# Kernel tuning notes

Hardware: AMD Instinct MI355X
Metric: run time of the kernel (lower is better)

The kernel has to match this reference:

```python
import jax, jax.numpy as jnp
import numpy as np

B, SD, SS = 2, 2048, 1024
H, NH, DH, FF = 768, 12, 64, 3072
L, V, P, NS, WIN = 6, 50265, 256, 32, 256


def layer_norm(x, g, b, eps=1e-5):
    m = x.mean(-1, keepdims=True)
    v = ((x - m) ** 2).mean(-1, keepdims=True)
    return (x - m) * jax.lax.rsqrt(v + eps) * g + b


def sliding_window_attention(q, k, v, key_mask, w):
    # q,k,v: [B,NH,S,DH]; key_mask: [B,S] (1 = attend); one-sided window w
    b, nh, s, d = q.shape
    nc = s // w
    qc = q.reshape(b, nh, nc, w, d)
    kp = jnp.pad(k, ((0, 0), (0, 0), (w, w), (0, 0)))
    vp = jnp.pad(v, ((0, 0), (0, 0), (w, w), (0, 0)))
    idx = jnp.arange(nc)[:, None] * w + jnp.arange(3 * w)[None, :]  # [nc,3w]
    kc = kp[:, :, idx]  # [B,NH,nc,3w,DH]
    vc = vp[:, :, idx]
    km = jnp.pad(key_mask, ((0, 0), (w, w)))[:, idx]  # [B,nc,3w]
    scores = jnp.einsum('bhcqd,bhckd->bhcqk', qc, kc) / np.float32(np.sqrt(d))
    rel = jnp.arange(3 * w)[None, :] - jnp.arange(w)[:, None]
    band = (rel >= 0) & (rel <= 2 * w)  # |j - i| <= w in global coords
    mask = band[None, None, None] & (km[:, None, :, None, :] > 0)
    probs = jax.nn.softmax(jnp.where(mask, scores, -1e9), axis=-1)
    return jnp.einsum('bhcqk,bhckd->bhcqd', probs, vc).reshape(b, nh, s, d)


def encode(ids, amask, word_emb, pos_emb, emb_g, emb_b, Wq, bq, Wk, bk, Wv, bv, Wo, bo,
           lnag, lnab, Wf1, bf1, Wf2, bf2, lnfg, lnfb):
    bb, s = ids.shape
    x = word_emb[ids] + pos_emb[:s][None]
    x = layer_norm(x, emb_g, emb_b)
    km = amask.astype(jnp.float32)
    for l in range(L):
        to_heads = lambda t: t.reshape(bb, s, NH, DH).transpose(0, 2, 1, 3)
        q = to_heads(x @ Wq[l] + bq[l])
        k = to_heads(x @ Wk[l] + bk[l])
        v = to_heads(x @ Wv[l] + bv[l])
        a = sliding_window_attention(q, k, v, km, WIN)
        a = a.transpose(0, 2, 1, 3).reshape(bb, s, H) @ Wo[l] + bo[l]
        x = layer_norm(x + a, lnag[l], lnab[l])
        h = jax.nn.gelu(x @ Wf1[l] + bf1[l], approximate=False) @ Wf2[l] + bf2[l]
        x = layer_norm(x + h, lnfg[l], lnfb[l])
    return x


def process_spans(seq_out, span_masks, pool_w, pj_g1, pj_b1, pj_W1, pj_c1, pj_g2, pj_b2, pj_W2, pj_c2):
    scores = jnp.clip(seq_out @ pool_w, -100.0, 100.0)  # [N,S]
    am = (span_masks == 1).astype(jnp.float32)
    scores = scores * am + (-1e9) * (1.0 - am)
    attn = jax.nn.softmax(scores, axis=-1)[..., None]
    emb = (seq_out * attn).sum(axis=1)  # [N,H]
    h = layer_norm(emb, pj_g1, pj_b1)
    h = jax.nn.gelu(h @ pj_W1 + pj_c1, approximate=False)
    h = layer_norm(h, pj_g2, pj_b2)
    proj = h @ pj_W2 + pj_c2
    n = jnp.maximum(jnp.linalg.norm(proj, axis=1, keepdims=True), 1e-12)
    return proj / n


def setup_inputs():
    key = jax.random.key(0)
    ks = jax.random.split(key, 40)
    nrm = lambda k, shape, s=0.02: (jax.random.normal(k, shape) * s).astype(jnp.float32)
    return {
        'doc_input_ids': jax.random.randint(ks[0], (B, SD), 0, V),
        'doc_attention_mask': jnp.ones((B, SD), jnp.int32),
        'summary_input_ids': jax.random.randint(ks[1], (B, SS), 0, V),
        'summary_attention_mask': jnp.ones((B, SS), jnp.int32),
        'og_span_masks': jax.random.randint(ks[2], (NS, SD), 0, 2),
        'llm_span_masks': jax.random.randint(ks[3], (NS, SS), 0, 2),
        'sample_indices': jax.random.randint(ks[4], (NS,), 0, B),
        'word_emb': nrm(ks[5], (V, H)),
        'pos_emb': nrm(ks[6], (SD, H)),
        'emb_g': jnp.ones((H,), jnp.float32), 'emb_b': jnp.zeros((H,), jnp.float32),
        'Wq': nrm(ks[7], (L, H, H)), 'bq': jnp.zeros((L, H), jnp.float32),
        'Wk': nrm(ks[8], (L, H, H)), 'bk': jnp.zeros((L, H), jnp.float32),
        'Wv': nrm(ks[9], (L, H, H)), 'bv': jnp.zeros((L, H), jnp.float32),
        'Wo': nrm(ks[10], (L, H, H)), 'bo': jnp.zeros((L, H), jnp.float32),
        'lnag': jnp.ones((L, H), jnp.float32), 'lnab': jnp.zeros((L, H), jnp.float32),
        'Wf1': nrm(ks[11], (L, H, FF)), 'bf1': jnp.zeros((L, FF), jnp.float32),
        'Wf2': nrm(ks[12], (L, FF, H)), 'bf2': jnp.zeros((L, H), jnp.float32),
        'lnfg': jnp.ones((L, H), jnp.float32), 'lnfb': jnp.zeros((L, H), jnp.float32),
        'pool_w': nrm(ks[13], (H,), 0.005),
        'pj_g1': jnp.ones((H,), jnp.float32), 'pj_b1': jnp.zeros((H,), jnp.float32),
        'pj_W1': nrm(ks[14], (H, H), 0.005), 'pj_c1': jnp.zeros((H,), jnp.float32),
        'pj_g2': jnp.ones((H,), jnp.float32), 'pj_b2': jnp.zeros((H,), jnp.float32),
        'pj_W2': nrm(ks[15], (H, P), 0.005), 'pj_c2': jnp.zeros((P,), jnp.float32),
    }


def reference(doc_input_ids, doc_attention_mask, summary_input_ids, summary_attention_mask,
              og_span_masks, llm_span_masks, sample_indices,
              word_emb, pos_emb, emb_g, emb_b, Wq, bq, Wk, bk, Wv, bv, Wo, bo,
              lnag, lnab, Wf1, bf1, Wf2, bf2, lnfg, lnfb,
              pool_w, pj_g1, pj_b1, pj_W1, pj_c1, pj_g2, pj_b2, pj_W2, pj_c2):
    enc = lambda ids, am: encode(ids, am, word_emb, pos_emb, emb_g, emb_b, Wq, bq, Wk, bk,
                                 Wv, bv, Wo, bo, lnag, lnab, Wf1, bf1, Wf2, bf2, lnfg, lnfb)
    doc_out = enc(doc_input_ids, doc_attention_mask)
    sum_out = enc(summary_input_ids, summary_attention_mask)
    human_seq = doc_out[sample_indices]  # [NS,SD,H]
    llm_seq = sum_out[sample_indices]    # [NS,SS,H]
    pj = (pool_w, pj_g1, pj_b1, pj_W1, pj_c1, pj_g2, pj_b2, pj_W2, pj_c2)
    human = process_spans(human_seq, og_span_masks, *pj)
    llm = process_spans(llm_seq, llm_span_masks, *pj)
    return (human, llm)
```

## Files before the change

### kernel.cpp

```cpp
#include <hip/hip_runtime.h>
#include <math.h>

#define BB 2
#define SDOC 2048
#define SSUM 1024
#define HD 768
#define NHEAD 12
#define DHEAD 64
#define FFD 3072
#define NLAYER 6
#define PD 256
#define NSPAN 32
#define WINSZ 256
#define QKVN 2304
#define MTOT 6144
#define KSPLIT 16

typedef short s16x8 __attribute__((ext_vector_type(8)));
typedef float f32x4 __attribute__((ext_vector_type(4)));

#define LDS_PTR(p) ((__attribute__((address_space(3))) void*)(p))
#define GLB_PTR(p) ((const __attribute__((address_space(1))) void*)(p))

__device__ __forceinline__ unsigned short f2bf(float f) {
  unsigned int u = __builtin_bit_cast(unsigned int, f);
  unsigned int r = (u + 0x7fffu + ((u >> 16) & 1u)) >> 16;
  return (unsigned short)r;
}
__device__ __forceinline__ float bf2f(unsigned short h) {
  unsigned int u = ((unsigned int)h) << 16;
  return __builtin_bit_cast(float, u);
}

__device__ __forceinline__ float gelu_f(float x) {
  float t = x * (0.7978845608f + 0.0356774081f * x * x);
  float e = __expf(2.f * t);
  float th = 1.f - 2.f / (e + 1.f);
  return 0.5f * x * (1.f + th);
}

__device__ __forceinline__ float wave_reduce_sum(float v) {
#pragma unroll
  for (int m = 32; m > 0; m >>= 1) v += __shfl_xor(v, m, 64);
  return v;
}
__device__ __forceinline__ float wave_reduce_max(float v) {
#pragma unroll
  for (int m = 32; m > 0; m >>= 1) v = fmaxf(v, __shfl_xor(v, m, 64));
  return v;
}

__device__ __forceinline__ float block_reduce_sum(float v) {
  __shared__ float s[4];
  v = wave_reduce_sum(v);
  int wave = threadIdx.x >> 6;
  if ((threadIdx.x & 63) == 0) s[wave] = v;
  __syncthreads();
  float r = (s[0] + s[1]) + (s[2] + s[3]);
  __syncthreads();
  return r;
}

__device__ __forceinline__ float block_reduce_max(float v) {
  __shared__ float s[4];
  v = wave_reduce_max(v);
  int wave = threadIdx.x >> 6;
  if ((threadIdx.x & 63) == 0) s[wave] = v;
  __syncthreads();
  float r = fmaxf(fmaxf(s[0], s[1]), fmaxf(s[2], s[3]));
  __syncthreads();
  return r;
}

__device__ __forceinline__ void block_reduce_sum2(float& a, float& b) {
  __shared__ float sa[4], sb[4];
#pragma unroll
  for (int m = 32; m > 0; m >>= 1) {
    a += __shfl_xor(a, m, 64);
    b += __shfl_xor(b, m, 64);
  }
  int wave = threadIdx.x >> 6;
  if ((threadIdx.x & 63) == 0) { sa[wave] = a; sb[wave] = b; }
  __syncthreads();
  a = (sa[0] + sa[1]) + (sa[2] + sa[3]);
  b = (sb[0] + sb[1]) + (sb[2] + sb[3]);
  __syncthreads();
}

__global__ __launch_bounds__(256) void embed_ln_kernel(
    const int* __restrict__ ids, const float* __restrict__ we, const float* __restrict__ pe,
    const float* __restrict__ g, const float* __restrict__ bt, float* __restrict__ xout,
    unsigned short* __restrict__ xb, int S) {
  int row = blockIdx.x;
  int s = row % S;
  int id = ids[row];
  int tid = threadIdx.x;
  float vals[3];
  float sum = 0.f, sq = 0.f;
#pragma unroll
  for (int i = 0; i < 3; i++) {
    int h = tid + i * 256;
    float t = we[(size_t)id * HD + h] + pe[(size_t)s * HD + h];
    vals[i] = t;
    sum += t;
    sq += t * t;
  }
  block_reduce_sum2(sum, sq);
  float mean = sum * (1.f / HD);
  float var = fmaxf(sq * (1.f / HD) - mean * mean, 0.f);
  float inv = rsqrtf(var + 1e-5f);
#pragma unroll
  for (int i = 0; i < 3; i++) {
    int h = tid + i * 256;
    float v = (vals[i] - mean) * inv * g[h] + bt[h];
    size_t off = (size_t)row * HD + h;
    xout[off] = v;
    xb[off] = f2bf(v);
  }
}

__global__ __launch_bounds__(256) void ln_kernel(
    const float* __restrict__ a, const float* __restrict__ res,
    const float* __restrict__ g, const float* __restrict__ bt, float* __restrict__ out,
    unsigned short* __restrict__ ob) {
  int row = blockIdx.x;
  int tid = threadIdx.x;
  const float* ar = a + (size_t)row * HD;
  const float* rr = res ? res + (size_t)row * HD : nullptr;
  float vals[3];
  float sum = 0.f, sq = 0.f;
#pragma unroll
  for (int i = 0; i < 3; i++) {
    int h = tid + i * 256;
    float t = ar[h] + (rr ? rr[h] : 0.f);
    vals[i] = t;
    sum += t;
    sq += t * t;
  }
  block_reduce_sum2(sum, sq);
  float mean = sum * (1.f / HD);
  float var = fmaxf(sq * (1.f / HD) - mean * mean, 0.f);
  float inv = rsqrtf(var + 1e-5f);
#pragma unroll
  for (int i = 0; i < 3; i++) {
    int h = tid + i * 256;
    float v = (vals[i] - mean) * inv * g[h] + bt[h];
    size_t off = (size_t)row * HD + h;
    out[off] = v;
    if (ob) ob[off] = f2bf(v);
  }
}

__global__ __launch_bounds__(256) void tc_cast_kernel(
    const float* __restrict__ Wq, const float* __restrict__ Wk, const float* __restrict__ Wv,
    const float* __restrict__ Wo, const float* __restrict__ Wf1, const float* __restrict__ Wf2,
    unsigned short* __restrict__ ob) {
  __shared__ float tile[32][33];
  int z = blockIdx.z;
  const float* W;
  int Kd, Nd;
  size_t off;
  switch (z) {
    case 0: W = Wq;  Kd = HD;  Nd = HD;  off = 0;        break;
    case 1: W = Wk;  Kd = HD;  Nd = HD;  off = 589824;   break;
    case 2: W = Wv;  Kd = HD;  Nd = HD;  off = 1179648;  break;
    case 3: W = Wo;  Kd = HD;  Nd = HD;  off = 1769472;  break;
    case 4: W = Wf1; Kd = HD;  Nd = FFD; off = 2359296;  break;
    default: W = Wf2; Kd = FFD; Nd = HD; off = 4718592;  break;
  }
  int tiles_n = Nd >> 5, tiles_k = Kd >> 5;
  int t = blockIdx.x;
  if (t >= tiles_n * tiles_k) return;
  int tn = t % tiles_n, tk = t / tiles_n;
  int n0 = tn * 32, k0 = tk * 32;
  int tid = threadIdx.x;
  int c = tid & 31, r0 = tid >> 5;
#pragma unroll
  for (int j = 0; j < 4; j++) {
    int r = r0 + j * 8;
    tile[r][c] = W[(size_t)(k0 + r) * Nd + n0 + c];
  }
  __syncthreads();
#pragma unroll
  for (int j = 0; j < 4; j++) {
    int r = r0 + j * 8;
    ob[off + (size_t)(n0 + r) * Kd + k0 + c] = f2bf(tile[c][r]);
  }
}

template <int TN>
__global__ __launch_bounds__(256) void gemm_mfma_t(
    const unsigned short* __restrict__ A, const unsigned short* __restrict__ B,
    const float* __restrict__ b0, const float* __restrict__ b1, const float* __restrict__ b2,
    int seg, float* __restrict__ C, unsigned short* __restrict__ Oh,
    int M, int N, int K, int act) {
  constexpr int JT = TN / 32;
  __shared__ __align__(16) unsigned short sA[2][128 * 32];
  __shared__ __align__(16) unsigned short sB[2][TN * 32];
  int tid = threadIdx.x;
  int bm = blockIdx.y * 128, bn = blockIdx.x * TN;
  int wave = tid >> 6, lane = tid & 63;
  int quad = lane >> 4, l16 = lane & 15;
  int wm = (wave >> 1) * 64, wn = (wave & 1) * (TN / 2);

  f32x4 zero = {0.f, 0.f, 0.f, 0.f};
  f32x4 acc[4][JT];
#pragma unroll
  for (int i = 0; i < 4; i++)
#pragma unroll
    for (int j = 0; j < JT; j++) acc[i][j] = zero;

  int e0 = tid * 8;
  int row0 = e0 >> 5;
  int kk0 = e0 & 31;

  auto issue = [&](int kb, int buf) {
    int k0 = kb * 32;
#pragma unroll
    for (int r = 0; r < 2; r++) {
      int row = row0 + r * 64;
      int le = (r * 256 + tid) * 8;
      size_t ga = (size_t)(bm + row) * K + k0 + kk0;
      __builtin_amdgcn_global_load_lds(GLB_PTR(A + ga), LDS_PTR(&sA[buf][le]), 16, 0, 0);
    }
#pragma unroll
    for (int r = 0; r < TN / 64; r++) {
      int row = row0 + r * 64;
      int le = (r * 256 + tid) * 8;
      size_t gb = (size_t)(bn + row) * K + k0 + kk0;
      __builtin_amdgcn_global_load_lds(GLB_PTR(B + gb), LDS_PTR(&sB[buf][le]), 16, 0, 0);
    }
  };

  int nk = K >> 5;
  issue(0, 0);
  for (int kb = 0; kb < nk; kb++) {
    __syncthreads();
    if (kb + 1 < nk) issue(kb + 1, (kb + 1) & 1);
    int buf = kb & 1;
    s16x8 af[4], bf[JT];
#pragma unroll
    for (int i = 0; i < 4; i++)
      af[i] = *(const s16x8*)&sA[buf][(wm + i * 16 + l16) * 32 + quad * 8];
#pragma unroll
    for (int j = 0; j < JT; j++)
      bf[j] = *(const s16x8*)&sB[buf][(wn + j * 16 + l16) * 32 + quad * 8];
#pragma unroll
    for (int i = 0; i < 4; i++)
#pragma unroll
      for (int j = 0; j < JT; j++)
        acc[i][j] = __builtin_amdgcn_mfma_f32_16x16x32_bf16(af[i], bf[j], acc[i][j], 0, 0, 0);
  }

#pragma unroll
  for (int j = 0; j < JT; j++) {
    int col = bn + wn + j * 16 + l16;
    int bidx = col / seg;
    int boff = col - bidx * seg;
    const float* bp = bidx == 0 ? b0 : (bidx == 1 ? b1 : b2);
    float bv = bp[boff];
#pragma unroll
    for (int i = 0; i < 4; i++) {
#pragma unroll
      for (int r = 0; r < 4; r++) {
        int rowg = bm + wm + i * 16 + quad * 4 + r;
        float v = acc[i][j][r] + bv;
        if (act == 1) v = gelu_f(v);
        size_t off = (size_t)rowg * N + col;
        if (C) C[off] = v;
        if (Oh) Oh[off] = f2bf(v);
      }
    }
  }
}

__global__ __launch_bounds__(256) void gemm_ps_kernel(
    const float* __restrict__ A, const float* __restrict__ W,
    float* __restrict__ part, int N, int K) {
  int n = blockIdx.x * 256 + threadIdx.x;
  int m = blockIdx.y;
  int M = gridDim.y;
  int ks = blockIdx.z;
  int kc = K / KSPLIT;
  int k0 = ks * kc;
  const float* ar = A + (size_t)m * K + k0;
  const float* wr = W + (size_t)k0 * N + n;
  float a0 = 0.f, a1 = 0.f, a2 = 0.f, a3 = 0.f;
  for (int k = 0; k < kc; k += 4) {
    a0 += ar[k]     * wr[(size_t)k * N];
    a1 += ar[k + 1] * wr[(size_t)(k + 1) * N];
    a2 += ar[k + 2] * wr[(size_t)(k + 2) * N];
    a3 += ar[k + 3] * wr[(size_t)(k + 3) * N];
  }
  part[((size_t)ks * M + m) * N + n] = (a0 + a1) + (a2 + a3);
}

__global__ __launch_bounds__(256) void gemm_reduce_kernel(
    const float* __restrict__ part, const float* __restrict__ bias,
    float* __restrict__ C, int N, int act) {
  int n = blockIdx.x * 256 + threadIdx.x;
  int m = blockIdx.y;
  int M = gridDim.y;
  float s = 0.f;
#pragma unroll
  for (int ks = 0; ks < KSPLIT; ks++) s += part[((size_t)ks * M + m) * N + n];
  s += bias[n];
  if (act == 1) s = gelu_f(s);
  C[(size_t)m * N + n] = s;
}

#define AQT 64
__global__ __launch_bounds__(256) void attn_mfma(
    const unsigned short* __restrict__ qkv, const int* __restrict__ amask,
    unsigned short* __restrict__ Oh, int S) {
  __shared__ unsigned short Vs[64][72];
  __shared__ unsigned short Ps[4][16][72];
  int b = blockIdx.z, hd = blockIdx.y;
  int p0 = blockIdx.x * AQT;
  int tid = threadIdx.x;
  int wave = tid >> 6, lane = tid & 63;
  int quad = lane >> 4, l16 = lane & 15;
  int kstart = p0 - WINSZ;
  const unsigned short* base = qkv + (size_t)(b * S) * QKVN + hd * DHEAD;

  s16x8 aq[2];
  {
    const unsigned short* qrow = base + (size_t)(p0 + wave * 16 + l16) * QKVN;
    aq[0] = *(const s16x8*)(qrow + quad * 8);
    aq[1] = *(const s16x8*)(qrow + 32 + quad * 8);
  }
  f32x4 o[4];
  f32x4 zero = {0.f, 0.f, 0.f, 0.f};
#pragma unroll
  for (int i = 0; i < 4; i++) o[i] = zero;
  float mi[4] = {-1e30f, -1e30f, -1e30f, -1e30f};
  float li[4] = {0.f, 0.f, 0.f, 0.f};

  for (int t = 0; t < 9; t++) {
    __syncthreads();
    {
      int key = tid & 63, d0 = (tid >> 6) * 16;
      int kp = kstart + t * 64 + key;
      if (kp >= 0 && kp < S) {
        const unsigned short* vrow = base + (size_t)kp * QKVN + 2 * HD + d0;
        s16x8 v0 = *(const s16x8*)(vrow);
        s16x8 v1 = *(const s16x8*)(vrow + 8);
#pragma unroll
        for (int j = 0; j < 8; j++) Vs[d0 + j][key] = (unsigned short)v0[j];
#pragma unroll
        for (int j = 0; j < 8; j++) Vs[d0 + 8 + j][key] = (unsigned short)v1[j];
      } else {
#pragma unroll
        for (int j = 0; j < 16; j++) Vs[d0 + j][key] = 0;
      }
    }
    __syncthreads();

    f32x4 sc[4];
#pragma unroll
    for (int nt = 0; nt < 4; nt++) {
      int kr = kstart + t * 64 + nt * 16 + l16;
      s16x8 bk0 = {0, 0, 0, 0, 0, 0, 0, 0}, bk1 = bk0;
      if (kr >= 0 && kr < S) {
        const unsigned short* krow = base + (size_t)kr * QKVN + HD;
        bk0 = *(const s16x8*)(krow + quad * 8);
        bk1 = *(const s16x8*)(krow + 32 + quad * 8);
      }
      sc[nt] = __builtin_amdgcn_mfma_f32_16x16x32_bf16(aq[0], bk0, zero, 0, 0, 0);
      sc[nt] = __builtin_amdgcn_mfma_f32_16x16x32_bf16(aq[1], bk1, sc[nt], 0, 0, 0);
    }

    float s_val[4][4];
    float tm[4] = {-1e30f, -1e30f, -1e30f, -1e30f};
#pragma unroll
    for (int nt = 0; nt < 4; nt++) {
      int j = t * 64 + nt * 16 + l16;
      int kp = kstart + j;
      int am = (kp >= 0 && kp < S) ? amask[b * S + kp] : 0;
#pragma unroll
      for (int r = 0; r < 4; r++) {
        int ql = wave * 16 + quad * 4 + r;
        bool valid = (am != 0) && (j >= ql) && (j <= ql + 512);
        float v = valid ? sc[nt][r] * 0.125f : -1e9f;
        s_val[nt][r] = v;
        tm[r] = fmaxf(tm[r], v);
      }
    }
#pragma unroll
    for (int m = 1; m < 16; m <<= 1)
#pragma unroll
      for (int r = 0; r < 4; r++) tm[r] = fmaxf(tm[r], __shfl_xor(tm[r], m, 16));

    float alpha[4], rs[4];
#pragma unroll
    for (int r = 0; r < 4; r++) {
      float mn = fmaxf(mi[r], tm[r]);
      alpha[r] = __expf(mi[r] - mn);
      mi[r] = mn;
      rs[r] = 0.f;
    }
#pragma unroll
    for (int nt = 0; nt < 4; nt++)
#pragma unroll
      for (int r = 0; r < 4; r++) {
        float p = __expf(s_val[nt][r] - mi[r]);
        rs[r] += p;
        Ps[wave][quad * 4 + r][nt * 16 + l16] = f2bf(p);
      }
#pragma unroll
    for (int m = 1; m < 16; m <<= 1)
#pragma unroll
      for (int r = 0; r < 4; r++) rs[r] += __shfl_xor(rs[r], m, 16);
#pragma unroll
    for (int r = 0; r < 4; r++) li[r] = li[r] * alpha[r] + rs[r];
#pragma unroll
    for (int dn = 0; dn < 4; dn++)
#pragma unroll
      for (int r = 0; r < 4; r++) o[dn][r] *= alpha[r];

#pragma unroll
    for (int ks = 0; ks < 2; ks++) {
      s16x8 ap = *(const s16x8*)&Ps[wave][l16][ks * 32 + quad * 8];
#pragma unroll
      for (int dn = 0; dn < 4; dn++) {
        s16x8 bv = *(const s16x8*)&Vs[dn * 16 + l16][ks * 32 + quad * 8];
        o[dn] = __builtin_amdgcn_mfma_f32_16x16x32_bf16(ap, bv, o[dn], 0, 0, 0);
      }
    }
  }

#pragma unroll
  for (int r = 0; r < 4; r++) {
    float inv = 1.f / li[r];
    int rowg = b * S + p0 + wave * 16 + quad * 4 + r;
#pragma unroll
    for (int dn = 0; dn < 4; dn++) {
      Oh[(size_t)rowg * HD + hd * DHEAD + dn * 16 + l16] = f2bf(o[dn][r] * inv);
    }
  }
}

__global__ __launch_bounds__(256) void dots_kernel(
    const float* __restrict__ x, const float* __restrict__ pw, float* __restrict__ dots) {
  int row = blockIdx.x * 4 + (threadIdx.x >> 6);
  int lane = threadIdx.x & 63;
  const float* r = x + (size_t)row * HD;
  float s = 0.f;
  for (int i = lane; i < HD; i += 64) s += r[i] * pw[i];
#pragma unroll
  for (int m = 32; m > 0; m >>= 1) s += __shfl_xor(s, m, 64);
  if (lane == 0) dots[row] = fminf(fmaxf(s, -100.f), 100.f);
}

__global__ __launch_bounds__(256) void span_softmax_kernel(
    const float* __restrict__ dots, const int* __restrict__ og_spans,
    const int* __restrict__ llm_spans, const int* __restrict__ sidx,
    float* __restrict__ probs) {
  int ns = blockIdx.x;
  int pass = ns >> 5;
  int sp = ns & 31;
  int S = pass ? SSUM : SDOC;
  const int* spans = pass ? llm_spans : og_spans;
  int rowbase = pass ? BB * SDOC : 0;
  int bi = sidx[sp];
  const float* dr = dots + rowbase + bi * S;
  int tid = threadIdx.x;
  float mx = -1e30f;
  for (int s = tid; s < S; s += 256) {
    float v = (spans[sp * S + s] == 1) ? dr[s] : -1e9f;
    mx = fmaxf(mx, v);
  }
  mx = block_reduce_max(mx);
  float sum = 0.f;
  for (int s = tid; s < S; s += 256) {
    float v = (spans[sp * S + s] == 1) ? dr[s] : -1e9f;
    float e = __expf(v - mx);
    probs[ns * SDOC + s] = e;
    sum += e;
  }
  sum = block_reduce_sum(sum);
  float inv = 1.f / sum;
  for (int s = tid; s < S; s += 256) probs[ns * SDOC + s] *= inv;
}

__global__ __launch_bounds__(256) void wsum_kernel(
    const float* __restrict__ seq, const float* __restrict__ probs,
    const int* __restrict__ sidx, float* __restrict__ pooled, int S, int ns0) {
  __shared__ float ps[256];
  int sp = blockIdx.y;
  int ns = ns0 + sp;
  int s0 = blockIdx.x * 256;
  int bi = sidx[sp];
  int tid = threadIdx.x;
  ps[tid] = probs[ns * SDOC + s0 + tid];
  __syncthreads();
  const float* xb = seq + ((size_t)bi * S + s0) * HD;
  float a0 = 0.f, a1 = 0.f, a2 = 0.f;
  for (int s = 0; s < 256; s++) {
    float p = ps[s];
    const float* row = xb + (size_t)s * HD;
    a0 += p * row[tid];
    a1 += p * row[tid + 256];
    a2 += p * row[tid + 512];
  }
  atomicAdd(&pooled[ns * HD + tid], a0);
  atomicAdd(&pooled[ns * HD + tid + 256], a1);
  atomicAdd(&pooled[ns * HD + tid + 512], a2);
}

__global__ __launch_bounds__(256) void norm_out_kernel(
    const float* __restrict__ proj, float* __restrict__ out) {
  int ns = blockIdx.x;
  float v = proj[ns * PD + threadIdx.x];
  float ss = block_reduce_sum(v * v);
  float n = fmaxf(sqrtf(ss), 1e-12f);
  out[ns * PD + threadIdx.x] = v / n;
}

static void launch_gemm128(const unsigned short* A, const unsigned short* B,
                           const float* b0, const float* b1, const float* b2, int seg,
                           float* C, unsigned short* Oh, int M, int N, int K, int act,
                           hipStream_t stream) {
  dim3 grid(N / 128, M / 128);
  gemm_mfma_t<128><<<grid, 256, 0, stream>>>(A, B, b0, b1, b2, seg, C, Oh, M, N, K, act);
}

#define WOFF_QKV 0
#define WOFF_O   1769472
#define WOFF_F1  2359296
#define WOFF_F2  4718592

extern "C" void kernel_launch(void* const* d_in, const int* in_sizes, int n_in,
                              void* d_out, int out_size, void* d_ws, size_t ws_size,
                              hipStream_t stream) {
  const int* doc_ids   = (const int*)d_in[0];
  const int* doc_am    = (const int*)d_in[1];
  const int* sum_ids   = (const int*)d_in[2];
  const int* sum_am    = (const int*)d_in[3];
  const int* og_spans  = (const int*)d_in[4];
  const int* llm_spans = (const int*)d_in[5];
  const int* sidx      = (const int*)d_in[6];
  const float* word_emb = (const float*)d_in[7];
  const float* pos_emb  = (const float*)d_in[8];
  const float* emb_g = (const float*)d_in[9];
  const float* emb_b = (const float*)d_in[10];
  const float* Wq = (const float*)d_in[11];
  const float* bq = (const float*)d_in[12];
  const float* Wk = (const float*)d_in[13];
  const float* bk = (const float*)d_in[14];
  const float* Wv = (const float*)d_in[15];
  const float* bv = (const float*)d_in[16];
  const float* Wo = (const float*)d_in[17];
  const float* bo = (const float*)d_in[18];
  const float* lnag = (const float*)d_in[19];
  const float* lnab = (const float*)d_in[20];
  const float* Wf1 = (const float*)d_in[21];
  const float* bf1 = (const float*)d_in[22];
  const float* Wf2 = (const float*)d_in[23];
  const float* bf2 = (const float*)d_in[24];
  const float* lnfg = (const float*)d_in[25];
  const float* lnfb = (const float*)d_in[26];
  const float* pool_w = (const float*)d_in[27];
  const float* pj_g1 = (const float*)d_in[28];
  const float* pj_b1 = (const float*)d_in[29];
  const float* pj_W1 = (const float*)d_in[30];
  const float* pj_c1 = (const float*)d_in[31];
  const float* pj_g2 = (const float*)d_in[32];
  const float* pj_b2 = (const float*)d_in[33];
  const float* pj_W2 = (const float*)d_in[34];
  const float* pj_c2 = (const float*)d_in[35];
  float* out = (float*)d_out;

  const size_t n_x = (size_t)MTOT * HD;
  float* x      = (float*)d_ws;
  float* cbuf   = x + n_x;
  float* pooled = cbuf + n_x;
  float* g1     = pooled + 2 * NSPAN * HD;
  float* h2     = g1 + 2 * NSPAN * HD;
  float* proj   = h2 + 2 * NSPAN * HD;
  float* dots   = proj + 2 * NSPAN * PD;
  float* probs  = dots + MTOT;
  float* pbuf   = probs + 2 * NSPAN * SDOC;
  unsigned short* xbf    = (unsigned short*)(pbuf + (size_t)KSPLIT * 2 * NSPAN * HD);
  unsigned short* qkv_bf = xbf + n_x;
  unsigned short* ab_bf  = qkv_bf + (size_t)MTOT * QKVN;
  unsigned short* h_bf   = ab_bf + n_x;
  unsigned short* wt_bf  = h_bf + (size_t)MTOT * FFD;

  embed_ln_kernel<<<BB * SDOC, 256, 0, stream>>>(doc_ids, word_emb, pos_emb, emb_g, emb_b,
                                                 x, xbf, SDOC);
  embed_ln_kernel<<<BB * SSUM, 256, 0, stream>>>(sum_ids, word_emb, pos_emb, emb_g, emb_b,
                                                 x + (size_t)BB * SDOC * HD,
                                                 xbf + (size_t)BB * SDOC * HD, SSUM);

  const size_t sum_off = (size_t)BB * SDOC;
  for (int l = 0; l < NLAYER; l++) {
    tc_cast_kernel<<<dim3(2304, 1, 6), 256, 0, stream>>>(
        Wq + (size_t)l * HD * HD, Wk + (size_t)l * HD * HD, Wv + (size_t)l * HD * HD,
        Wo + (size_t)l * HD * HD, Wf1 + (size_t)l * HD * FFD, Wf2 + (size_t)l * FFD * HD,
        wt_bf);
    launch_gemm128(xbf, wt_bf + WOFF_QKV, bq + l * HD, bk + l * HD, bv + l * HD, HD,
                   nullptr, qkv_bf, MTOT, QKVN, HD, 0, stream);
    attn_mfma<<<dim3(SDOC / AQT, NHEAD, BB), 256, 0, stream>>>(qkv_bf, doc_am, ab_bf, SDOC);
    attn_mfma<<<dim3(SSUM / AQT, NHEAD, BB), 256, 0, stream>>>(
        qkv_bf + sum_off * QKVN, sum_am, ab_bf + sum_off * HD, SSUM);
    launch_gemm128(ab_bf, wt_bf + WOFF_O, bo + l * HD, bo + l * HD, bo + l * HD, HD,
                   cbuf, nullptr, MTOT, HD, HD, 0, stream);
    ln_kernel<<<MTOT, 256, 0, stream>>>(cbuf, x, lnag + l * HD, lnab + l * HD, x, xbf);
    launch_gemm128(xbf, wt_bf + WOFF_F1, bf1 + l * FFD, bf1 + l * FFD, bf1 + l * FFD, FFD,
                   nullptr, h_bf, MTOT, FFD, HD, 1, stream);
    launch_gemm128(h_bf, wt_bf + WOFF_F2, bf2 + l * HD, bf2 + l * HD, bf2 + l * HD, HD,
                   cbuf, nullptr, MTOT, HD, FFD, 0, stream);
    ln_kernel<<<MTOT, 256, 0, stream>>>(cbuf, x, lnfg + l * HD, lnfb + l * HD, x, xbf);
  }

  dots_kernel<<<MTOT / 4, 256, 0, stream>>>(x, pool_w, dots);
  span_softmax_kernel<<<2 * NSPAN, 256, 0, stream>>>(dots, og_spans, llm_spans, sidx, probs);
  hipMemsetAsync(pooled, 0, 2 * NSPAN * HD * sizeof(float), stream);
  wsum_kernel<<<dim3(SDOC / 256, NSPAN), 256, 0, stream>>>(x, probs, sidx, pooled, SDOC, 0);
  wsum_kernel<<<dim3(SSUM / 256, NSPAN), 256, 0, stream>>>(
      x + sum_off * HD, probs, sidx, pooled, SSUM, NSPAN);
  ln_kernel<<<2 * NSPAN, 256, 0, stream>>>(pooled, nullptr, pj_g1, pj_b1, h2, nullptr);
  gemm_ps_kernel<<<dim3(HD / 256, 2 * NSPAN, KSPLIT), 256, 0, stream>>>(h2, pj_W1, pbuf, HD, HD);
  gemm_reduce_kernel<<<dim3(HD / 256, 2 * NSPAN), 256, 0, stream>>>(pbuf, pj_c1, g1, HD, 1);
  ln_kernel<<<2 * NSPAN, 256, 0, stream>>>(g1, nullptr, pj_g2, pj_b2, h2, nullptr);
  gemm_ps_kernel<<<dim3(PD / 256, 2 * NSPAN, KSPLIT), 256, 0, stream>>>(h2, pj_W2, pbuf, PD, HD);
  gemm_reduce_kernel<<<dim3(PD / 256, 2 * NSPAN), 256, 0, stream>>>(pbuf, pj_c2, proj, PD, 0);
  norm_out_kernel<<<2 * NSPAN, 256, 0, stream>>>(proj, out);
}
```

Before: 2.489 ms.

## Split-K the O-proj and FF2 GEMMs and reduce partials inside LayerNorm

The two GEMMs with N=768 now launch with a K-split of two, each slice writing fp32 partials to separate buffers. The LayerNorm kernel is extended to sum both partials, the residual and the bias before normalizing, which fuses the split-K reduction and bias add into it. This is meant to fix poor CU occupancy from the small 288-block grid, at the cost of an extra fp32 partial buffer write and read.

Result: slower. 2.560 ms (+2.9%).

```diff
diff --git a/kernel.cpp b/kernel.cpp
--- a/kernel.cpp
+++ b/kernel.cpp
@@ -120,19 +120,24 @@
 }
 
 __global__ __launch_bounds__(256) void ln_kernel(
-    const float* __restrict__ a, const float* __restrict__ res,
+    const float* __restrict__ a, const float* __restrict__ a2,
+    const float* __restrict__ res, const float* __restrict__ bias,
     const float* __restrict__ g, const float* __restrict__ bt, float* __restrict__ out,
     unsigned short* __restrict__ ob) {
   int row = blockIdx.x;
   int tid = threadIdx.x;
   const float* ar = a + (size_t)row * HD;
+  const float* a2r = a2 ? a2 + (size_t)row * HD : nullptr;
   const float* rr = res ? res + (size_t)row * HD : nullptr;
   float vals[3];
   float sum = 0.f, sq = 0.f;
 #pragma unroll
   for (int i = 0; i < 3; i++) {
     int h = tid + i * 256;
-    float t = ar[h] + (rr ? rr[h] : 0.f);
+    float t = ar[h];
+    if (a2r) t += a2r[h];
+    if (rr) t += rr[h];
+    if (bias) t += bias[h];
     vals[i] = t;
     sum += t;
     sq += t * t;
@@ -199,6 +204,9 @@
   __shared__ __align__(16) unsigned short sB[2][TN * 32];
   int tid = threadIdx.x;
   int bm = blockIdx.y * 128, bn = blockIdx.x * TN;
+  int kz = blockIdx.z;
+  int KC = K / gridDim.z;
+  int kbase = kz * KC;
   int wave = tid >> 6, lane = tid & 63;
   int quad = lane >> 4, l16 = lane & 15;
   int wm = (wave >> 1) * 64, wn = (wave & 1) * (TN / 2);
@@ -215,7 +223,7 @@
   int kk0 = e0 & 31;
 
   auto issue = [&](int kb, int buf) {
-    int k0 = kb * 32;
+    int k0 = kbase + kb * 32;
 #pragma unroll
     for (int r = 0; r < 2; r++) {
       int row = row0 + r * 64;
@@ -232,7 +240,7 @@
     }
   };
 
-  int nk = K >> 5;
+  int nk = KC >> 5;
   issue(0, 0);
   for (int kb = 0; kb < nk; kb++) {
     __syncthreads();
@@ -250,6 +258,22 @@
 #pragma unroll
       for (int j = 0; j < JT; j++)
         acc[i][j] = __builtin_amdgcn_mfma_f32_16x16x32_bf16(af[i], bf[j], acc[i][j], 0, 0, 0);
+  }
+
+  if (gridDim.z > 1) {
+    float* Cp = C + (size_t)kz * M * N;
+#pragma unroll
+    for (int j = 0; j < JT; j++) {
+      int col = bn + wn + j * 16 + l16;
+#pragma unroll
+      for (int i = 0; i < 4; i++)
+#pragma unroll
+        for (int r = 0; r < 4; r++) {
+          int rowg = bm + wm + i * 16 + quad * 4 + r;
+          Cp[(size_t)rowg * N + col] = acc[i][j][r];
+        }
+    }
+    return;
   }
 
 #pragma unroll
@@ -523,6 +547,12 @@
                            hipStream_t stream) {
   dim3 grid(N / 128, M / 128);
   gemm_mfma_t<128><<<grid, 256, 0, stream>>>(A, B, b0, b1, b2, seg, C, Oh, M, N, K, act);
+}
+static void launch_gemm128_sk2(const unsigned short* A, const unsigned short* B,
+                               float* C, int M, int N, int K, hipStream_t stream) {
+  dim3 grid(N / 128, M / 128, 2);
+  gemm_mfma_t<128><<<grid, 256, 0, stream>>>(A, B, nullptr, nullptr, nullptr, N, C, nullptr,
+                                             M, N, K, 0);
 }
 
 #define WOFF_QKV 0
@@ -574,7 +604,8 @@
   const size_t n_x = (size_t)MTOT * HD;
   float* x      = (float*)d_ws;
   float* cbuf   = x + n_x;
-  float* pooled = cbuf + n_x;
+  float* cbuf2  = cbuf + n_x;
+  float* pooled = cbuf2 + n_x;
   float* g1     = pooled + 2 * NSPAN * HD;
   float* h2     = g1 + 2 * NSPAN * HD;
   float* proj   = h2 + 2 * NSPAN * HD;
@@ -604,14 +635,14 @@
     attn_mfma<<<dim3(SDOC / AQT, NHEAD, BB), 256, 0, stream>>>(qkv_bf, doc_am, ab_bf, SDOC);
     attn_mfma<<<dim3(SSUM / AQT, NHEAD, BB), 256, 0, stream>>>(
         qkv_bf + sum_off * QKVN, sum_am, ab_bf + sum_off * HD, SSUM);
-    launch_gemm128(ab_bf, wt_bf + WOFF_O, bo + l * HD, bo + l * HD, bo + l * HD, HD,
-                   cbuf, nullptr, MTOT, HD, HD, 0, stream);
-    ln_kernel<<<MTOT, 256, 0, stream>>>(cbuf, x, lnag + l * HD, lnab + l * HD, x, xbf);
+    launch_gemm128_sk2(ab_bf, wt_bf + WOFF_O, cbuf, MTOT, HD, HD, stream);
+    ln_kernel<<<MTOT, 256, 0, stream>>>(cbuf, cbuf2, x, bo + l * HD,
+                                        lnag + l * HD, lnab + l * HD, x, xbf);
     launch_gemm128(xbf, wt_bf + WOFF_F1, bf1 + l * FFD, bf1 + l * FFD, bf1 + l * FFD, FFD,
                    nullptr, h_bf, MTOT, FFD, HD, 1, stream);
-    launch_gemm128(h_bf, wt_bf + WOFF_F2, bf2 + l * HD, bf2 + l * HD, bf2 + l * HD, HD,
-                   cbuf, nullptr, MTOT, HD, FFD, 0, stream);
-    ln_kernel<<<MTOT, 256, 0, stream>>>(cbuf, x, lnfg + l * HD, lnfb + l * HD, x, xbf);
+    launch_gemm128_sk2(h_bf, wt_bf + WOFF_F2, cbuf, MTOT, HD, FFD, stream);
+    ln_kernel<<<MTOT, 256, 0, stream>>>(cbuf, cbuf2, x, bf2 + l * HD,
+                                        lnfg + l * HD, lnfb + l * HD, x, xbf);
   }
 
   dots_kernel<<<MTOT / 4, 256, 0, stream>>>(x, pool_w, dots);
@@ -620,10 +651,12 @@
   wsum_kernel<<<dim3(SDOC / 256, NSPAN), 256, 0, stream>>>(x, probs, sidx, pooled, SDOC, 0);
   wsum_kernel<<<dim3(SSUM / 256, NSPAN), 256, 0, stream>>>(
       x + sum_off * HD, probs, sidx, pooled, SSUM, NSPAN);
-  ln_kernel<<<2 * NSPAN, 256, 0, stream>>>(pooled, nullptr, pj_g1, pj_b1, h2, nullptr);
+  ln_kernel<<<2 * NSPAN, 256, 0, stream>>>(pooled, nullptr, nullptr, nullptr,
+                                           pj_g1, pj_b1, h2, nullptr);
   gemm_ps_kernel<<<dim3(HD / 256, 2 * NSPAN, KSPLIT), 256, 0, stream>>>(h2, pj_W1, pbuf, HD, HD);
   gemm_reduce_kernel<<<dim3(HD / 256, 2 * NSPAN), 256, 0, stream>>>(pbuf, pj_c1, g1, HD, 1);
-  ln_kernel<<<2 * NSPAN, 256, 0, stream>>>(g1, nullptr, pj_g2, pj_b2, h2, nullptr);
+  ln_kernel<<<2 * NSPAN, 256, 0, stream>>>(g1, nullptr, nullptr, nullptr,
+                                           pj_g2, pj_b2, h2, nullptr);
   gemm_ps_kernel<<<dim3(PD / 256, 2 * NSPAN, KSPLIT), 256, 0, stream>>>(h2, pj_W2, pbuf, PD, HD);
   gemm_reduce_kernel<<<dim3(PD / 256, 2 * NSPAN), 256, 0, stream>>>(pbuf, pj_c2, proj, PD, 0);
   norm_out_kernel<<<2 * NSPAN, 256, 0, stream>>>(proj, out);
```

## Batch weight casts, merge doc/summary launches, prefetch V tiles in attention

Applied to the files above, without the earlier changes.

Casts all layers' weights to bf16 in a single launch before the layer loop, using per-layer workspace offsets. It merges the doc and summary embedding launches, and the two attention launches, into one grid each. The attention kernel now issues the global load for the next V tile before the current tile's compute, holding it in registers. This cuts launch count and idle gaps between small kernels, and overlaps V load latency with compute. In exchange it needs a larger workspace for six layers of bf16 weights and uses more registers in the attention kernel.

Result: slower. 2.642 ms (+6.2%).

```diff
diff --git a/kernel.cpp b/kernel.cpp
--- a/kernel.cpp
+++ b/kernel.cpp
@@ -15,6 +15,7 @@
 #define QKVN 2304
 #define MTOT 6144
 #define KSPLIT 16
+#define WSTRIDE 7077888
 
 typedef short s16x8 __attribute__((ext_vector_type(8)));
 typedef float f32x4 __attribute__((ext_vector_type(4)));
@@ -88,12 +89,14 @@
 }
 
 __global__ __launch_bounds__(256) void embed_ln_kernel(
-    const int* __restrict__ ids, const float* __restrict__ we, const float* __restrict__ pe,
+    const int* __restrict__ doc_ids, const int* __restrict__ sum_ids,
+    const float* __restrict__ we, const float* __restrict__ pe,
     const float* __restrict__ g, const float* __restrict__ bt, float* __restrict__ xout,
-    unsigned short* __restrict__ xb, int S) {
+    unsigned short* __restrict__ xb) {
   int row = blockIdx.x;
-  int s = row % S;
-  int id = ids[row];
+  int id, s;
+  if (row < BB * SDOC) { s = row % SDOC; id = doc_ids[row]; }
+  else { int r2 = row - BB * SDOC; s = r2 % SSUM; id = sum_ids[r2]; }
   int tid = threadIdx.x;
   float vals[3];
   float sum = 0.f, sq = 0.f;
@@ -120,19 +123,24 @@
 }
 
 __global__ __launch_bounds__(256) void ln_kernel(
-    const float* __restrict__ a, const float* __restrict__ res,
+    const float* __restrict__ a, const float* __restrict__ a2,
+    const float* __restrict__ res, const float* __restrict__ bias,
     const float* __restrict__ g, const float* __restrict__ bt, float* __restrict__ out,
     unsigned short* __restrict__ ob) {
   int row = blockIdx.x;
   int tid = threadIdx.x;
   const float* ar = a + (size_t)row * HD;
+  const float* a2r = a2 ? a2 + (size_t)row * HD : nullptr;
   const float* rr = res ? res + (size_t)row * HD : nullptr;
   float vals[3];
   float sum = 0.f, sq = 0.f;
 #pragma unroll
   for (int i = 0; i < 3; i++) {
     int h = tid + i * 256;
-    float t = ar[h] + (rr ? rr[h] : 0.f);
+    float t = ar[h];
+    if (a2r) t += a2r[h];
+    if (rr) t += rr[h];
+    if (bias) t += bias[h];
     vals[i] = t;
     sum += t;
     sq += t * t;
@@ -157,17 +165,19 @@
     unsigned short* __restrict__ ob) {
   __shared__ float tile[32][33];
   int z = blockIdx.z;
+  int l = z / 6, w = z % 6;
   const float* W;
   int Kd, Nd;
   size_t off;
-  switch (z) {
-    case 0: W = Wq;  Kd = HD;  Nd = HD;  off = 0;        break;
-    case 1: W = Wk;  Kd = HD;  Nd = HD;  off = 589824;   break;
-    case 2: W = Wv;  Kd = HD;  Nd = HD;  off = 1179648;  break;
-    case 3: W = Wo;  Kd = HD;  Nd = HD;  off = 1769472;  break;
-    case 4: W = Wf1; Kd = HD;  Nd = FFD; off = 2359296;  break;
-    default: W = Wf2; Kd = FFD; Nd = HD; off = 4718592;  break;
-  }
+  switch (w) {
+    case 0: W = Wq  + (size_t)l * HD * HD;  Kd = HD;  Nd = HD;  off = 0;        break;
+    case 1: W = Wk  + (size_t)l * HD * HD;  Kd = HD;  Nd = HD;  off = 589824;   break;
+    case 2: W = Wv  + (size_t)l * HD * HD;  Kd = HD;  Nd = HD;  off = 1179648;  break;
+    case 3: W = Wo  + (size_t)l * HD * HD;  Kd = HD;  Nd = HD;  off = 1769472;  break;
+    case 4: W = Wf1 + (size_t)l * HD * FFD; Kd = HD;  Nd = FFD; off = 2359296;  break;
+    default: W = Wf2 + (size_t)l * FFD * HD; Kd = FFD; Nd = HD; off = 4718592;  break;
+  }
+  off += (size_t)l * WSTRIDE;
   int tiles_n = Nd >> 5, tiles_k = Kd >> 5;
   int t = blockIdx.x;
   if (t >= tiles_n * tiles_k) return;
@@ -311,17 +321,24 @@
 
 #define AQT 64
 __global__ __launch_bounds__(256) void attn_mfma(
-    const unsigned short* __restrict__ qkv, const int* __restrict__ amask,
-    unsigned short* __restrict__ Oh, int S) {
+    const unsigned short* __restrict__ qkv, const int* __restrict__ doc_am,
+    const int* __restrict__ sum_am, unsigned short* __restrict__ Oh) {
   __shared__ unsigned short Vs[64][72];
   __shared__ unsigned short Ps[4][16][72];
+  int bx = blockIdx.x;
   int b = blockIdx.z, hd = blockIdx.y;
-  int p0 = blockIdx.x * AQT;
+  int S, p0;
+  const int* amask;
+  size_t rowoff;
+  if (bx < SDOC / AQT) { S = SDOC; p0 = bx * AQT; amask = doc_am; rowoff = 0; }
+  else { S = SSUM; p0 = (bx - SDOC / AQT) * AQT; amask = sum_am; rowoff = (size_t)BB * SDOC; }
+  amask += b * S;
   int tid = threadIdx.x;
   int wave = tid >> 6, lane = tid & 63;
   int quad = lane >> 4, l16 = lane & 15;
   int kstart = p0 - WINSZ;
-  const unsigned short* base = qkv + (size_t)(b * S) * QKVN + hd * DHEAD;
+  const unsigned short* base = qkv + (rowoff + (size_t)b * S) * QKVN + hd * DHEAD;
+  unsigned short* obase = Oh + (rowoff + (size_t)b * S) * HD + hd * DHEAD;
 
   s16x8 aq[2];
   {
@@ -336,24 +353,32 @@
   float mi[4] = {-1e30f, -1e30f, -1e30f, -1e30f};
   float li[4] = {0.f, 0.f, 0.f, 0.f};
 
+  int vkey = tid & 63, vd0 = (tid >> 6) * 16;
+  s16x8 pv0 = {0, 0, 0, 0, 0, 0, 0, 0}, pv1 = pv0;
+  bool pvalid = false;
+  auto loadV = [&](int t) {
+    int kp = kstart + t * 64 + vkey;
+    pvalid = (kp >= 0 && kp < S);
+    if (pvalid) {
+      const unsigned short* vrow = base + (size_t)kp * QKVN + 2 * HD + vd0;
+      pv0 = *(const s16x8*)(vrow);
+      pv1 = *(const s16x8*)(vrow + 8);
+    }
+  };
+  loadV(0);
+
   for (int t = 0; t < 9; t++) {
     __syncthreads();
-    {
-      int key = tid & 63, d0 = (tid >> 6) * 16;
-      int kp = kstart + t * 64 + key;
-      if (kp >= 0 && kp < S) {
-        const unsigned short* vrow = base + (size_t)kp * QKVN + 2 * HD + d0;
-        s16x8 v0 = *(const s16x8*)(vrow);
-        s16x8 v1 = *(const s16x8*)(vrow + 8);
-#pragma unroll
-        for (int j = 0; j < 8; j++) Vs[d0 + j][key] = (unsigned short)v0[j];
-#pragma unroll
-        for (int j = 0; j < 8; j++) Vs[d0 + 8 + j][key] = (unsigned short)v1[j];
-      } else {
-#pragma unroll
-        for (int j = 0; j < 16; j++) Vs[d0 + j][key] = 0;
-      }
-    }
+    if (pvalid) {
+#pragma unroll
+      for (int j = 0; j < 8; j++) Vs[vd0 + j][vkey] = (unsigned short)pv0[j];
+#pragma unroll
+      for (int j = 0; j < 8; j++) Vs[vd0 + 8 + j][vkey] = (unsigned short)pv1[j];
+    } else {
+#pragma unroll
+      for (int j = 0; j < 16; j++) Vs[vd0 + j][vkey] = 0;
+    }
+    if (t < 8) loadV(t + 1);
     __syncthreads();
 
     f32x4 sc[4];
@@ -376,7 +401,7 @@
     for (int nt = 0; nt < 4; nt++) {
       int j = t * 64 + nt * 16 + l16;
       int kp = kstart + j;
-      int am = (kp >= 0 && kp < S) ? amask[b * S + kp] : 0;
+      int am = (kp >= 0 && kp < S) ? amask[kp] : 0;
 #pragma unroll
       for (int r = 0; r < 4; r++) {
         int ql = wave * 16 + quad * 4 + r;
@@ -432,10 +457,10 @@
 #pragma unroll
   for (int r = 0; r < 4; r++) {
     float inv = 1.f / li[r];
-    int rowg = b * S + p0 + wave * 16 + quad * 4 + r;
+    int rowl = p0 + wave * 16 + quad * 4 + r;
 #pragma unroll
     for (int dn = 0; dn < 4; dn++) {
-      Oh[(size_t)rowg * HD + hd * DHEAD + dn * 16 + l16] = f2bf(o[dn][r] * inv);
+      obase[(size_t)rowl * HD + dn * 16 + l16] = f2bf(o[dn][r] * inv);
     }
   }
 }
@@ -587,43 +612,42 @@
   unsigned short* h_bf   = ab_bf + n_x;
   unsigned short* wt_bf  = h_bf + (size_t)MTOT * FFD;
 
-  embed_ln_kernel<<<BB * SDOC, 256, 0, stream>>>(doc_ids, word_emb, pos_emb, emb_g, emb_b,
-                                                 x, xbf, SDOC);
-  embed_ln_kernel<<<BB * SSUM, 256, 0, stream>>>(sum_ids, word_emb, pos_emb, emb_g, emb_b,
-                                                 x + (size_t)BB * SDOC * HD,
-                                                 xbf + (size_t)BB * SDOC * HD, SSUM);
+  embed_ln_kernel<<<MTOT, 256, 0, stream>>>(doc_ids, sum_ids, word_emb, pos_emb,
+                                            emb_g, emb_b, x, xbf);
+  tc_cast_kernel<<<dim3(2304, 1, 6 * NLAYER), 256, 0, stream>>>(
+      Wq, Wk, Wv, Wo, Wf1, Wf2, wt_bf);
+
+  for (int l = 0; l < NLAYER; l++) {
+    const unsigned short* wt = wt_bf + (size_t)l * WSTRIDE;
+    launch_gemm128(xbf, wt + WOFF_QKV, bq + l * HD, bk + l * HD, bv + l * HD, HD,
+                   nullptr, qkv_bf, MTOT, QKVN, HD, 0, stream);
+    attn_mfma<<<dim3(SDOC / AQT + SSUM / AQT, NHEAD, BB), 256, 0, stream>>>(
+        qkv_bf, doc_am, sum_am, ab_bf);
+    launch_gemm128(ab_bf, wt + WOFF_O, bo + l * HD, bo + l * HD, bo + l * HD, HD,
+                   cbuf, nullptr, MTOT, HD, HD, 0, stream);
+    ln_kernel<<<MTOT, 256, 0, stream>>>(cbuf, nullptr, x, nullptr,
+                                        lnag + l * HD, lnab + l * HD, x, xbf);
+    launch_gemm128(xbf, wt + WOFF_F1, bf1 + l * FFD, bf1 + l * FFD, bf1 + l * FFD, FFD,
+                   nullptr, h_bf, MTOT, FFD, HD, 1, stream);
+    launch_gemm128(h_bf, wt + WOFF_F2, bf2 + l * HD, bf2 + l * HD, bf2 + l * HD, HD,
+                   cbuf, nullptr, MTOT, HD, FFD, 0, stream);
+    ln_kernel<<<MTOT, 256, 0, stream>>>(cbuf, nullptr, x, nullptr,
+                                        lnfg + l * HD, lnfb + l * HD, x, xbf);
+  }
 
   const size_t sum_off = (size_t)BB * SDOC;
-  for (int l = 0; l < NLAYER; l++) {
-    tc_cast_kernel<<<dim3(2304, 1, 6), 256, 0, stream>>>(
-        Wq + (size_t)l * HD * HD, Wk + (size_t)l * HD * HD, Wv + (size_t)l * HD * HD,
-        Wo + (size_t)l * HD * HD, Wf1 + (size_t)l * HD * FFD, Wf2 + (size_t)l * FFD * HD,
-        wt_bf);
-    launch_gemm128(xbf, wt_bf + WOFF_QKV, bq + l * HD, bk + l * HD, bv + l * HD, HD,
-                   nullptr, qkv_bf, MTOT, QKVN, HD, 0, stream);
-    attn_mfma<<<dim3(SDOC / AQT, NHEAD, BB), 256, 0, stream>>>(qkv_bf, doc_am, ab_bf, SDOC);
-    attn_mfma<<<dim3(SSUM / AQT, NHEAD, BB), 256, 0, stream>>>(
-        qkv_bf + sum_off * QKVN, sum_am, ab_bf + sum_off * HD, SSUM);
-    launch_gemm128(ab_bf, wt_bf + WOFF_O, bo + l * HD, bo + l * HD, bo + l * HD, HD,
-                   cbuf, nullptr, MTOT, HD, HD, 0, stream);
-    ln_kernel<<<MTOT, 256, 0, stream>>>(cbuf, x, lnag + l * HD, lnab + l * HD, x, xbf);
-    launch_gemm128(xbf, wt_bf + WOFF_F1, bf1 + l * FFD, bf1 + l * FFD, bf1 + l * FFD, FFD,
-                   nullptr, h_bf, MTOT, FFD, HD, 1, stream);
-    launch_gemm128(h_bf, wt_bf + WOFF_F2, bf2 + l * HD, bf2 + l * HD, bf2 + l * HD, HD,
-                   cbuf, nullptr, MTOT, HD, FFD, 0, stream);
-    ln_kernel<<<MTOT, 256, 0, stream>>>(cbuf, x, lnfg + l * HD, lnfb + l * HD, x, xbf);
-  }
-
   dots_kernel<<<MTOT / 4, 256, 0, stream>>>(x, pool_w, dots);
   span_softmax_kernel<<<2 * NSPAN, 256, 0, stream>>>(dots, og_spans, llm_spans, sidx, probs);
   hipMemsetAsync(pooled, 0, 2 * NSPAN * HD * sizeof(float), stream);
   wsum_kernel<<<dim3(SDOC / 256, NSPAN), 256, 0, stream>>>(x, probs, sidx, pooled, SDOC, 0);
   wsum_kernel<<<dim3(SSUM / 256, NSPAN), 256, 0, stream>>>(
       x + sum_off * HD, probs, sidx, pooled, SSUM, NSPAN);
-  ln_kernel<<<2 * NSPAN, 256, 0, stream>>>(pooled, nullptr, pj_g1, pj_b1, h2, nullptr);
+  ln_kernel<<<2 * NSPAN, 256, 0, stream>>>(pooled, nullptr, nullptr, nullptr,
+                                           pj_g1, pj_b1, h2, nullptr);
   gemm_ps_kernel<<<dim3(HD / 256, 2 * NSPAN, KSPLIT), 256, 0, stream>>>(h2, pj_W1, pbuf, HD, HD);
   gemm_reduce_kernel<<<dim3(HD / 256, 2 * NSPAN), 256, 0, stream>>>(pbuf, pj_c1, g1, HD, 1);
-  ln_kernel<<<2 * NSPAN, 256, 0, stream>>>(g1, nullptr, pj_g2, pj_b2, h2, nullptr);
+  ln_kernel<<<2 * NSPAN, 256, 0, stream>>>(g1, nullptr, nullptr, nullptr,
+                                           pj_g2, pj_b2, h2, nullptr);
   gemm_ps_kernel<<<dim3(PD / 256, 2 * NSPAN, KSPLIT), 256, 0, stream>>>(h2, pj_W2, pbuf, PD, HD);
   gemm_reduce_kernel<<<dim3(PD / 256, 2 * NSPAN), 256, 0, stream>>>(pbuf, pj_c2, proj, PD, 0);
   norm_out_kernel<<<2 * NSPAN, 256, 0, stream>>>(proj, out);
```
